# Kernel tuning notes

Measured on AMD Instinct MI355X. Metric: run time of the kernel, lower is better.

Reference implementation:

```python
import jax, jax.numpy as jnp
import numpy as np

NUM_AGENTS = 8
OBSERVATION_SIZE = 30
INPUT_SHAPE = 4 + 2 * OBSERVATION_SIZE  # 64
STATE_SHAPE = INPUT_SHAPE * NUM_AGENTS  # 512
HYPER_HIDDEN_DIM = 40
QMIX_HIDDEN_DIM = 40


def setup_inputs() -> dict:
    key = jax.random.key(0)
    ks = jax.random.split(key, 16)
    E, T = 256, 256

    def lin(k, fan_in, fan_out):
        kw, kb = jax.random.split(k)
        bound = 1.0 / np.sqrt(fan_in)
        w = jax.random.uniform(kw, (fan_in, fan_out), jnp.float32, -bound, bound)
        b = jax.random.uniform(kb, (fan_out,), jnp.float32, -bound, bound)
        return w, b

    hw1_w0, hw1_b0 = lin(ks[0], STATE_SHAPE, HYPER_HIDDEN_DIM)
    hw1_w1, hw1_b1 = lin(ks[1], HYPER_HIDDEN_DIM, NUM_AGENTS * QMIX_HIDDEN_DIM)
    hw2_w0, hw2_b0 = lin(ks[2], STATE_SHAPE, HYPER_HIDDEN_DIM)
    hw2_w1, hw2_b1 = lin(ks[3], HYPER_HIDDEN_DIM, QMIX_HIDDEN_DIM)
    hb1_w, hb1_b = lin(ks[4], STATE_SHAPE, QMIX_HIDDEN_DIM)
    hb2_w0, hb2_b0 = lin(ks[5], STATE_SHAPE, QMIX_HIDDEN_DIM)
    hb2_w1, hb2_b1 = lin(ks[6], QMIX_HIDDEN_DIM, 1)

    return {
        "q_values": jax.random.normal(ks[7], (E, T, NUM_AGENTS), jnp.float32),
        "states": jax.random.normal(ks[8], (E, T, STATE_SHAPE), jnp.float32),
        "hw1_w0": hw1_w0, "hw1_b0": hw1_b0, "hw1_w1": hw1_w1, "hw1_b1": hw1_b1,
        "hw2_w0": hw2_w0, "hw2_b0": hw2_b0, "hw2_w1": hw2_w1, "hw2_b1": hw2_b1,
        "hb1_w": hb1_w, "hb1_b": hb1_b,
        "hb2_w0": hb2_w0, "hb2_b0": hb2_b0, "hb2_w1": hb2_w1, "hb2_b1": hb2_b1,
    }


def reference(q_values, states, hw1_w0, hw1_b0, hw1_w1, hw1_b1,
              hw2_w0, hw2_b0, hw2_w1, hw2_b1,
              hb1_w, hb1_b, hb2_w0, hb2_b0, hb2_w1, hb2_b1):
    E = q_values.shape[0]
    q = q_values.reshape(-1, NUM_AGENTS)          # [B, A]
    s = states.reshape(-1, STATE_SHAPE)           # [B, S]

    # hyper_w1: Linear-ReLU-Linear -> abs -> [B, A, H]
    w1 = jnp.abs(jax.nn.relu(s @ hw1_w0 + hw1_b0) @ hw1_w1 + hw1_b1)
    w1 = w1.reshape(-1, NUM_AGENTS, QMIX_HIDDEN_DIM)
    b1 = s @ hb1_w + hb1_b                        # [B, H]

    hidden = jax.nn.elu(jnp.einsum('ba,bah->bh', q, w1) + b1)  # [B, H]

    # hyper_w2 -> abs -> [B, H]; hyper_b2 -> [B, 1]
    w2 = jnp.abs(jax.nn.relu(s @ hw2_w0 + hw2_b0) @ hw2_w1 + hw2_b1)
    b2 = jax.nn.relu(s @ hb2_w0 + hb2_b0) @ hb2_w1 + hb2_b1    # [B, 1]

    q_total = jnp.einsum('bh,bh->b', hidden, w2)[:, None] + b2  # [B, 1]
    return q_total.reshape(E, -1, 1)
```

## Files before the change

kernel.cpp:

```cpp
#include <hip/hip_runtime.h>
#include <math.h>

#define NA 8
#define SS 512
#define BROWS 32
#define NTHREADS 320

typedef __attribute__((ext_vector_type(8))) short bf16x8;
typedef __attribute__((ext_vector_type(4))) float f32x4;

static __device__ __forceinline__ unsigned short f2bf(float f) {
    union { float f; unsigned u; } v; v.f = f;
    unsigned r = v.u + 0x7FFFu + ((v.u >> 16) & 1u);
    return (unsigned short)(r >> 16);
}
static __device__ __forceinline__ float bf2f(unsigned short u) {
    union { unsigned u; float f; } v; v.u = ((unsigned)u) << 16; return v.f;
}

#define BP_OFF   0
#define BP1_OFF  81920
#define BP2_OFF  102400
#define BIAS0_BYTE 210944

__global__ void prep_kernel(const float* __restrict__ hw1_w0, const float* __restrict__ hb1_w,
                            const float* __restrict__ hw2_w0, const float* __restrict__ hb2_w0,
                            const float* __restrict__ hw1_w1, const float* __restrict__ hw2_w1,
                            const float* __restrict__ hw1_b0, const float* __restrict__ hb1_b,
                            const float* __restrict__ hw2_b0, const float* __restrict__ hb2_b0,
                            unsigned short* __restrict__ ws16, float* __restrict__ bias0) {
    int idx = blockIdx.x * blockDim.x + threadIdx.x;
    if (idx < 81920) {
        int i = idx & 7, l = (idx >> 3) & 63, t = idx >> 9;
        int kt = t & 15, nt = t >> 4;
        int k = kt * 32 + (l >> 4) * 8 + i;
        int n = nt * 16 + (l & 15);
        int seg = n / 40, c = n - seg * 40;
        const float* src = (seg == 0) ? hw1_w0 : (seg == 1) ? hb1_w : (seg == 2) ? hw2_w0 : hb2_w0;
        ws16[BP_OFF + idx] = f2bf(src[k * 40 + c]);
    } else if (idx < 81920 + 20480) {
        int j = idx - 81920;
        int i = j & 7, l = (j >> 3) & 63, t = j >> 9;
        int kt = t & 1, nt = t >> 1;
        int k = kt * 32 + (l >> 4) * 8 + i;
        int n = nt * 16 + (l & 15);
        float v = (k < 40) ? hw1_w1[k * 320 + n] : 0.f;
        ws16[BP1_OFF + j] = f2bf(v);
    } else if (idx < 81920 + 20480 + 3072) {
        int j = idx - 102400;
        int i = j & 7, l = (j >> 3) & 63, t = j >> 9;
        int kt = t & 1, nt = t >> 1;
        int k = kt * 32 + (l >> 4) * 8 + i;
        int n = nt * 16 + (l & 15);
        float v = (k < 40 && n < 40) ? hw2_w1[k * 40 + n] : 0.f;
        ws16[BP2_OFF + j] = f2bf(v);
    } else if (idx < 81920 + 20480 + 3072 + 160) {
        int j = idx - 105472;
        int seg = j / 40, c = j - seg * 40;
        const float* b = (seg == 0) ? hw1_b0 : (seg == 1) ? hb1_b : (seg == 2) ? hw2_b0 : hb2_b0;
        bias0[j] = b[c];
    }
}

#define W1_STRIDE 324
#define B1_OFF    32768
#define H1_OFF    38400
#define H2_OFF    42496
#define W2_OFF    46592
#define B2_OFF    49152
#define SMEM_BYTES 49408

__global__ __launch_bounds__(NTHREADS, 4) void qmix_kernel(
    const float* __restrict__ q_values, const float* __restrict__ states,
    const unsigned short* __restrict__ Bp, const unsigned short* __restrict__ Bp1,
    const unsigned short* __restrict__ Bp2, const float* __restrict__ bias0,
    const float* __restrict__ hw1_b1, const float* __restrict__ hw2_b1,
    const float* __restrict__ hb2_w1, const float* __restrict__ hb2_b1,
    float* __restrict__ out)
{
    __shared__ __align__(16) char smem[SMEM_BYTES];
    const int tid = threadIdx.x;
    const int wv = tid >> 6;
    const int l = tid & 63;
    const int p = l & 15;
    const int row0 = blockIdx.x * BROWS;

    {
        const float4* sg = (const float4*)(states + (size_t)row0 * SS);
        for (int idx = tid; idx < BROWS * (SS / 4); idx += NTHREADS) {
            int r = idx >> 7;
            int c4 = idx & 127;
            float4 v = sg[idx];
            ushort4 b;
            b.x = f2bf(v.x); b.y = f2bf(v.y); b.z = f2bf(v.z); b.w = f2bf(v.w);
            int byte = (r * 1024 + c4 * 8) ^ ((r & 7) << 4);
            *(ushort4*)(smem + byte) = b;
        }
        for (int idx = tid; idx < 32 * 24; idx += NTHREADS) {
            int r = idx / 24, k = 40 + (idx - r * 24);
            int byte = (r * 128 + k * 2) ^ ((r & 7) << 4);
            *(unsigned short*)(smem + H1_OFF + byte) = 0;
            *(unsigned short*)(smem + H2_OFF + byte) = 0;
        }
    }
    __syncthreads();

    f32x4 acc[2][2] = {};
    {
        const int kch = (l >> 4) * 16;
        const int r0 = p;
        const int r1 = r0 + 16;
        const int swz0 = (r0 & 7) << 4;
        const unsigned short* bp0 = Bp + (size_t)((wv * 2 + 0) * 16) * 512 + (size_t)l * 8;
        const unsigned short* bp1 = Bp + (size_t)((wv * 2 + 1) * 16) * 512 + (size_t)l * 8;
        #pragma unroll
        for (int kt = 0; kt < 16; ++kt) {
            bf16x8 a0 = *(const bf16x8*)(smem + ((r0 * 1024 + kt * 64 + kch) ^ swz0));
            bf16x8 a1 = *(const bf16x8*)(smem + ((r1 * 1024 + kt * 64 + kch) ^ swz0));
            bf16x8 b0 = *(const bf16x8*)(bp0 + kt * 512);
            bf16x8 b1 = *(const bf16x8*)(bp1 + kt * 512);
            acc[0][0] = __builtin_amdgcn_mfma_f32_16x16x32_bf16(a0, b0, acc[0][0], 0, 0, 0);
            acc[0][1] = __builtin_amdgcn_mfma_f32_16x16x32_bf16(a0, b1, acc[0][1], 0, 0, 0);
            acc[1][0] = __builtin_amdgcn_mfma_f32_16x16x32_bf16(a1, b0, acc[1][0], 0, 0, 0);
            acc[1][1] = __builtin_amdgcn_mfma_f32_16x16x32_bf16(a1, b1, acc[1][1], 0, 0, 0);
        }
    }

    {
        float rs[2][4] = {{0.f,0.f,0.f,0.f},{0.f,0.f,0.f,0.f}};
        float* b1buf = (float*)(smem + B1_OFF);
        #pragma unroll
        for (int ntl = 0; ntl < 2; ++ntl) {
            const int c = wv * 32 + ntl * 16 + p;
            const float bia = bias0[c];
            const float hbw = (c >= 120) ? hb2_w1[c - 120] : 0.f;
            #pragma unroll
            for (int mt = 0; mt < 2; ++mt)
            #pragma unroll
            for (int g = 0; g < 4; ++g) {
                const int row = mt * 16 + (l >> 4) * 4 + g;
                const float v = acc[mt][ntl][g] + bia;
                if (c < 40) {
                    *(unsigned short*)(smem + H1_OFF + ((row * 128 + c * 2) ^ ((row & 7) << 4)))
                        = f2bf(fmaxf(v, 0.f));
                } else if (c < 80) {
                    b1buf[row * 44 + (c - 40)] = v;
                } else if (c < 120) {
                    *(unsigned short*)(smem + H2_OFF + ((row * 128 + (c - 80) * 2) ^ ((row & 7) << 4)))
                        = f2bf(fmaxf(v, 0.f));
                } else {
                    rs[mt][g] += fmaxf(v, 0.f) * hbw;
                }
            }
        }
        if (wv >= 3) {
            float* B2 = (float*)(smem + B2_OFF);
            #pragma unroll
            for (int mt = 0; mt < 2; ++mt)
            #pragma unroll
            for (int g = 0; g < 4; ++g) {
                float r2 = rs[mt][g];
                r2 += __shfl_xor(r2, 1);
                r2 += __shfl_xor(r2, 2);
                r2 += __shfl_xor(r2, 4);
                r2 += __shfl_xor(r2, 8);
                if (p == 0) B2[(wv - 3) * 32 + mt * 16 + (l >> 4) * 4 + g] = r2;
            }
        }
    }
    __syncthreads();

    {
        char* H1 = smem + H1_OFF;
        const int kch = (l >> 4) * 16;
        f32x4 wacc[2][4] = {};
        #pragma unroll
        for (int kt = 0; kt < 2; ++kt) {
            bf16x8 a[2];
            #pragma unroll
            for (int mt = 0; mt < 2; ++mt) {
                int row = mt * 16 + p;
                a[mt] = *(const bf16x8*)(H1 + ((row * 128 + kt * 64 + kch) ^ ((row & 7) << 4)));
            }
            #pragma unroll
            for (int t = 0; t < 4; ++t) {
                int nt1 = wv * 4 + t;
                bf16x8 b = *(const bf16x8*)(Bp1 + ((size_t)(nt1 * 2 + kt) * 64 + l) * 8);
                wacc[0][t] = __builtin_amdgcn_mfma_f32_16x16x32_bf16(a[0], b, wacc[0][t], 0, 0, 0);
                wacc[1][t] = __builtin_amdgcn_mfma_f32_16x16x32_bf16(a[1], b, wacc[1][t], 0, 0, 0);
            }
        }
        unsigned short* W1 = (unsigned short*)smem;
        #pragma unroll
        for (int mt = 0; mt < 2; ++mt)
        #pragma unroll
        for (int t = 0; t < 4; ++t)
        #pragma unroll
        for (int g = 0; g < 4; ++g) {
            int row = mt * 16 + (l >> 4) * 4 + g;
            int n = (wv * 4 + t) * 16 + p;
            W1[row * W1_STRIDE + n] = f2bf(fabsf(wacc[mt][t][g] + hw1_b1[n]));
        }
        if (wv < 3) {
            char* H2 = smem + H2_OFF;
            f32x4 c2[2] = {};
            #pragma unroll
            for (int kt = 0; kt < 2; ++kt) {
                bf16x8 a[2];
                #pragma unroll
                for (int mt = 0; mt < 2; ++mt) {
                    int row = mt * 16 + p;
                    a[mt] = *(const bf16x8*)(H2 + ((row * 128 + kt * 64 + kch) ^ ((row & 7) << 4)));
                }
                bf16x8 b = *(const bf16x8*)(Bp2 + ((size_t)(wv * 2 + kt) * 64 + l) * 8);
                c2[0] = __builtin_amdgcn_mfma_f32_16x16x32_bf16(a[0], b, c2[0], 0, 0, 0);
                c2[1] = __builtin_amdgcn_mfma_f32_16x16x32_bf16(a[1], b, c2[1], 0, 0, 0);
            }
            unsigned short* W2 = (unsigned short*)(smem + W2_OFF);
            #pragma unroll
            for (int mt = 0; mt < 2; ++mt)
            #pragma unroll
            for (int g = 0; g < 4; ++g) {
                int row = mt * 16 + (l >> 4) * 4 + g;
                int n = wv * 16 + p;
                if (n < 40) W2[row * 40 + n] = f2bf(fabsf(c2[mt][g] + hw2_b1[n]));
            }
        }
    }
    __syncthreads();

    {
        float* b1buf = (float*)(smem + B1_OFF);
        unsigned short* W1 = (unsigned short*)smem;
        unsigned short* W2 = (unsigned short*)(smem + W2_OFF);
        float* PR = (float*)(smem + H1_OFF);
        int r = tid / 10;
        int hb_ = tid - r * 10;
        const float4* qp = (const float4*)(q_values + (size_t)(row0 + r) * NA);
        float4 qa = qp[0], qb = qp[1];
        float qv[8] = {qa.x, qa.y, qa.z, qa.w, qb.x, qb.y, qb.z, qb.w};
        float psum = 0.f;
        #pragma unroll
        for (int kk = 0; kk < 4; ++kk) {
            int h = hb_ + kk * 10;
            float acc2 = b1buf[r * 44 + h];
            #pragma unroll
            for (int a = 0; a < 8; ++a) acc2 += qv[a] * bf2f(W1[r * W1_STRIDE + a * 40 + h]);
            float hid = (acc2 > 0.f) ? acc2 : expm1f(acc2);
            psum += hid * bf2f(W2[r * 40 + h]);
        }
        PR[tid] = psum;
    }
    __syncthreads();
    if (tid < 32) {
        float* PR = (float*)(smem + H1_OFF);
        float* B2 = (float*)(smem + B2_OFF);
        float s = B2[tid] + B2[32 + tid] + hb2_b1[0];
        #pragma unroll
        for (int g = 0; g < 10; ++g) s += PR[tid * 10 + g];
        out[row0 + tid] = s;
    }
}

extern "C" void kernel_launch(void* const* d_in, const int* in_sizes, int n_in,
                              void* d_out, int out_size, void* d_ws, size_t ws_size,
                              hipStream_t stream) {
    const float* q_values = (const float*)d_in[0];
    const float* states   = (const float*)d_in[1];
    const float* hw1_w0 = (const float*)d_in[2];
    const float* hw1_b0 = (const float*)d_in[3];
    const float* hw1_w1 = (const float*)d_in[4];
    const float* hw1_b1 = (const float*)d_in[5];
    const float* hw2_w0 = (const float*)d_in[6];
    const float* hw2_b0 = (const float*)d_in[7];
    const float* hw2_w1 = (const float*)d_in[8];
    const float* hw2_b1 = (const float*)d_in[9];
    const float* hb1_w  = (const float*)d_in[10];
    const float* hb1_b  = (const float*)d_in[11];
    const float* hb2_w0 = (const float*)d_in[12];
    const float* hb2_b0 = (const float*)d_in[13];
    const float* hb2_w1 = (const float*)d_in[14];
    const float* hb2_b1 = (const float*)d_in[15];

    unsigned short* ws16 = (unsigned short*)d_ws;
    float* bias0 = (float*)((char*)d_ws + BIAS0_BYTE);

    const int prep_total = 81920 + 20480 + 3072 + 160;
    prep_kernel<<<(prep_total + 255) / 256, 256, 0, stream>>>(
        hw1_w0, hb1_w, hw2_w0, hb2_w0, hw1_w1, hw2_w1,
        hw1_b0, hb1_b, hw2_b0, hb2_b0, ws16, bias0);

    const int B = in_sizes[0] / NA;
    qmix_kernel<<<B / BROWS, NTHREADS, 0, stream>>>(
        q_values, states,
        ws16 + BP_OFF, ws16 + BP1_OFF, ws16 + BP2_OFF, bias0,
        hw1_b1, hw2_b1, hb2_w1, hb2_b1, (float*)d_out);
}
```

Measured before the change: 268.7 us.

## Load states directly from global into MFMA operands, drop LDS staging

```diff
diff --git a/kernel.cpp b/kernel.cpp
--- a/kernel.cpp
+++ b/kernel.cpp
@@ -8,6 +8,7 @@
 
 typedef __attribute__((ext_vector_type(8))) short bf16x8;
 typedef __attribute__((ext_vector_type(4))) float f32x4;
+typedef __attribute__((ext_vector_type(4))) unsigned u32x4;
 
 static __device__ __forceinline__ unsigned short f2bf(float f) {
     union { float f; unsigned u; } v; v.f = f;
@@ -16,6 +17,17 @@
 }
 static __device__ __forceinline__ float bf2f(unsigned short u) {
     union { unsigned u; float f; } v; v.u = ((unsigned)u) << 16; return v.f;
+}
+static __device__ __forceinline__ unsigned pk2(float lo, float hi) {
+    return (unsigned)f2bf(lo) | ((unsigned)f2bf(hi) << 16);
+}
+static __device__ __forceinline__ bf16x8 cvt8(float4 a, float4 b) {
+    u32x4 t;
+    t[0] = pk2(a.x, a.y);
+    t[1] = pk2(a.z, a.w);
+    t[2] = pk2(b.x, b.y);
+    t[3] = pk2(b.z, b.w);
+    return __builtin_bit_cast(bf16x8, t);
 }
 
 #define BP_OFF   0
@@ -63,12 +75,13 @@
 }
 
 #define W1_STRIDE 324
-#define B1_OFF    32768
-#define H1_OFF    38400
-#define H2_OFF    42496
-#define W2_OFF    46592
-#define B2_OFF    49152
-#define SMEM_BYTES 49408
+#define W1_OFF    0
+#define B1_OFF    20736
+#define H1_OFF    26496
+#define H2_OFF    30592
+#define W2_OFF    34688
+#define B2_OFF    37248
+#define SMEM_BYTES 37504
 
 __global__ __launch_bounds__(NTHREADS, 4) void qmix_kernel(
     const float* __restrict__ q_values, const float* __restrict__ states,
@@ -85,40 +98,44 @@
     const int p = l & 15;
     const int row0 = blockIdx.x * BROWS;
 
-    {
-        const float4* sg = (const float4*)(states + (size_t)row0 * SS);
-        for (int idx = tid; idx < BROWS * (SS / 4); idx += NTHREADS) {
-            int r = idx >> 7;
-            int c4 = idx & 127;
-            float4 v = sg[idx];
-            ushort4 b;
-            b.x = f2bf(v.x); b.y = f2bf(v.y); b.z = f2bf(v.z); b.w = f2bf(v.w);
-            int byte = (r * 1024 + c4 * 8) ^ ((r & 7) << 4);
-            *(ushort4*)(smem + byte) = b;
-        }
-        for (int idx = tid; idx < 32 * 24; idx += NTHREADS) {
-            int r = idx / 24, k = 40 + (idx - r * 24);
-            int byte = (r * 128 + k * 2) ^ ((r & 7) << 4);
-            *(unsigned short*)(smem + H1_OFF + byte) = 0;
-            *(unsigned short*)(smem + H2_OFF + byte) = 0;
-        }
-    }
-    __syncthreads();
+    const int rq = tid & 31;
+    const float4* qp = (const float4*)(q_values + (size_t)(row0 + rq) * NA);
+    float4 qa = qp[0], qb = qp[1];
+
+    const int c0 = wv * 32 + p, c1 = c0 + 16;
+    const float bia0v = bias0[c0], bia1v = bias0[c1];
+    const float hbw0 = (c0 >= 120) ? hb2_w1[c0 - 120] : 0.f;
+    const float hbw1 = (c1 >= 120) ? hb2_w1[c1 - 120] : 0.f;
+    float hb1v[4];
+    #pragma unroll
+    for (int t = 0; t < 4; ++t) hb1v[t] = hw1_b1[(wv * 4 + t) * 16 + p];
+    const int n2 = wv * 16 + p;
+    const float hb2v = (n2 < 40) ? hw2_b1[n2] : 0.f;
+    const float hb2b = hb2_b1[0];
+
+    for (int idx = tid; idx < 32 * 24; idx += NTHREADS) {
+        int r = idx / 24, k = 40 + (idx - r * 24);
+        int byte = (r * 128 + k * 2) ^ ((r & 7) << 4);
+        *(unsigned short*)(smem + H1_OFF + byte) = 0;
+        *(unsigned short*)(smem + H2_OFF + byte) = 0;
+    }
 
     f32x4 acc[2][2] = {};
     {
-        const int kch = (l >> 4) * 16;
-        const int r0 = p;
-        const int r1 = r0 + 16;
-        const int swz0 = (r0 & 7) << 4;
+        const float* Arow0 = states + (size_t)(row0 + p) * SS + (l >> 4) * 8;
+        const float* Arow1 = Arow0 + 16 * SS;
         const unsigned short* bp0 = Bp + (size_t)((wv * 2 + 0) * 16) * 512 + (size_t)l * 8;
         const unsigned short* bp1 = Bp + (size_t)((wv * 2 + 1) * 16) * 512 + (size_t)l * 8;
         #pragma unroll
         for (int kt = 0; kt < 16; ++kt) {
-            bf16x8 a0 = *(const bf16x8*)(smem + ((r0 * 1024 + kt * 64 + kch) ^ swz0));
-            bf16x8 a1 = *(const bf16x8*)(smem + ((r1 * 1024 + kt * 64 + kch) ^ swz0));
+            float4 x0 = *(const float4*)(Arow0 + kt * 32);
+            float4 x1 = *(const float4*)(Arow0 + kt * 32 + 4);
+            float4 y0 = *(const float4*)(Arow1 + kt * 32);
+            float4 y1 = *(const float4*)(Arow1 + kt * 32 + 4);
             bf16x8 b0 = *(const bf16x8*)(bp0 + kt * 512);
             bf16x8 b1 = *(const bf16x8*)(bp1 + kt * 512);
+            bf16x8 a0 = cvt8(x0, x1);
+            bf16x8 a1 = cvt8(y0, y1);
             acc[0][0] = __builtin_amdgcn_mfma_f32_16x16x32_bf16(a0, b0, acc[0][0], 0, 0, 0);
             acc[0][1] = __builtin_amdgcn_mfma_f32_16x16x32_bf16(a0, b1, acc[0][1], 0, 0, 0);
             acc[1][0] = __builtin_amdgcn_mfma_f32_16x16x32_bf16(a1, b0, acc[1][0], 0, 0, 0);
@@ -132,8 +149,8 @@
         #pragma unroll
         for (int ntl = 0; ntl < 2; ++ntl) {
             const int c = wv * 32 + ntl * 16 + p;
-            const float bia = bias0[c];
-            const float hbw = (c >= 120) ? hb2_w1[c - 120] : 0.f;
+            const float bia = ntl ? bia1v : bia0v;
+            const float hbw = ntl ? hbw1 : hbw0;
             #pragma unroll
             for (int mt = 0; mt < 2; ++mt)
             #pragma unroll
@@ -144,7 +161,7 @@
                     *(unsigned short*)(smem + H1_OFF + ((row * 128 + c * 2) ^ ((row & 7) << 4)))
                         = f2bf(fmaxf(v, 0.f));
                 } else if (c < 80) {
-                    b1buf[row * 44 + (c - 40)] = v;
+                    b1buf[row * 45 + (c - 40)] = v;
                 } else if (c < 120) {
                     *(unsigned short*)(smem + H2_OFF + ((row * 128 + (c - 80) * 2) ^ ((row & 7) << 4)))
                         = f2bf(fmaxf(v, 0.f));
@@ -190,7 +207,7 @@
                 wacc[1][t] = __builtin_amdgcn_mfma_f32_16x16x32_bf16(a[1], b, wacc[1][t], 0, 0, 0);
             }
         }
-        unsigned short* W1 = (unsigned short*)smem;
+        unsigned short* W1 = (unsigned short*)(smem + W1_OFF);
         #pragma unroll
         for (int mt = 0; mt < 2; ++mt)
         #pragma unroll
@@ -199,7 +216,7 @@
         for (int g = 0; g < 4; ++g) {
             int row = mt * 16 + (l >> 4) * 4 + g;
             int n = (wv * 4 + t) * 16 + p;
-            W1[row * W1_STRIDE + n] = f2bf(fabsf(wacc[mt][t][g] + hw1_b1[n]));
+            W1[row * W1_STRIDE + n] = f2bf(fabsf(wacc[mt][t][g] + hb1v[t]));
         }
         if (wv < 3) {
             char* H2 = smem + H2_OFF;
@@ -223,7 +240,7 @@
             for (int g = 0; g < 4; ++g) {
                 int row = mt * 16 + (l >> 4) * 4 + g;
                 int n = wv * 16 + p;
-                if (n < 40) W2[row * 40 + n] = f2bf(fabsf(c2[mt][g] + hw2_b1[n]));
+                if (n < 40) W2[row * 40 + n] = f2bf(fabsf(c2[mt][g] + hb2v));
             }
         }
     }
@@ -231,19 +248,17 @@
 
     {
         float* b1buf = (float*)(smem + B1_OFF);
-        unsigned short* W1 = (unsigned short*)smem;
+        unsigned short* W1 = (unsigned short*)(smem + W1_OFF);
         unsigned short* W2 = (unsigned short*)(smem + W2_OFF);
         float* PR = (float*)(smem + H1_OFF);
-        int r = tid / 10;
-        int hb_ = tid - r * 10;
-        const float4* qp = (const float4*)(q_values + (size_t)(row0 + r) * NA);
-        float4 qa = qp[0], qb = qp[1];
+        const int r = tid & 31;
+        const int gq = tid >> 5;
         float qv[8] = {qa.x, qa.y, qa.z, qa.w, qb.x, qb.y, qb.z, qb.w};
         float psum = 0.f;
         #pragma unroll
         for (int kk = 0; kk < 4; ++kk) {
-            int h = hb_ + kk * 10;
-            float acc2 = b1buf[r * 44 + h];
+            int h = gq * 4 + kk;
+            float acc2 = b1buf[r * 45 + h];
             #pragma unroll
             for (int a = 0; a < 8; ++a) acc2 += qv[a] * bf2f(W1[r * W1_STRIDE + a * 40 + h]);
             float hid = (acc2 > 0.f) ? acc2 : expm1f(acc2);
@@ -255,9 +270,9 @@
     if (tid < 32) {
         float* PR = (float*)(smem + H1_OFF);
         float* B2 = (float*)(smem + B2_OFF);
-        float s = B2[tid] + B2[32 + tid] + hb2_b1[0];
-        #pragma unroll
-        for (int g = 0; g < 10; ++g) s += PR[tid * 10 + g];
+        float s = B2[tid] + B2[32 + tid] + hb2b;
+        #pragma unroll
+        for (int g = 0; g < 10; ++g) s += PR[g * 32 + tid];
         out[row0 + tid] = s;
     }
 }
```

Measured after the change: 294.7 us. 1.1x slower.
